# Optimization experiments

Measured on AMD Instinct MI355X. Metric: run time of the kernel, lower is better.

Reference implementation:

```python
import jax, jax.numpy as jnp
import numpy as np

INPUT_DIM = 1024
HIDDEN = 64
NUM_MEM = 8   # +1 shared slot -> 9 total
K = 2
SEQ = 256
BATCH = 32


def setup_inputs() -> dict:
    key = jax.random.key(0)
    ks = jax.random.split(key, 10)
    s = 1.0 / np.sqrt(INPUT_DIM)
    nm1 = NUM_MEM + 1
    return {
        "X": jax.random.normal(ks[0], (SEQ, BATCH, INPUT_DIM), jnp.float32),
        "M_0": jnp.zeros((BATCH, nm1, HIDDEN, HIDDEN), jnp.float32),
        "Wk_w": jax.random.uniform(ks[1], (HIDDEN * nm1, INPUT_DIM), jnp.float32, -s, s),
        "Wk_b": jax.random.uniform(ks[2], (HIDDEN * nm1,), jnp.float32, -s, s),
        "Wv_w": jax.random.uniform(ks[3], (HIDDEN * nm1, INPUT_DIM), jnp.float32, -s, s),
        "Wv_b": jax.random.uniform(ks[4], (HIDDEN * nm1,), jnp.float32, -s, s),
        "Wg_w": jax.random.uniform(ks[5], (NUM_MEM, INPUT_DIM), jnp.float32, -s, s),
        "Wg_b": jax.random.uniform(ks[6], (NUM_MEM,), jnp.float32, -s, s),
        "Wq_w": jax.random.uniform(ks[7], (HIDDEN, INPUT_DIM), jnp.float32, -s, s),
        "Wq_b": jax.random.uniform(ks[8], (HIDDEN,), jnp.float32, -s, s),
    }


def _mom_forward(X, M_0, Wk_w, Wk_b, Wv_w, Wv_b, Wg_w, Wg_b, Wq_w, Wq_b):
    B = X.shape[1]
    nm1 = NUM_MEM + 1
    b_idx = jnp.arange(B)[:, None]

    def step(M, x_t):
        # gating + top-k routing (sorted descending, like torch.topk)
        score = jax.nn.softmax(x_t @ Wg_w.T + Wg_b, axis=1)          # (B, NUM_MEM)
        m_scores, m_idx = jax.lax.top_k(score, K)                    # (B, K)
        idx_update = jnp.concatenate(
            [jnp.zeros((B, 1), jnp.int32), m_idx.astype(jnp.int32)], axis=1)  # (B, K+1)
        g = m_scores / jnp.sum(m_scores, axis=1, keepdims=True)     # (B, K)

        Mk = (x_t @ Wk_w.T + Wk_b).reshape(B, nm1, HIDDEN)          # (B, 9, H)
        Mv = (x_t @ Wv_w.T + Wv_b).reshape(B, nm1, HIDDEN)
        # only gather the K+1 routed outer products instead of all 9
        k_sel = jnp.take_along_axis(Mk, idx_update[:, :, None], axis=1)  # (B, K+1, H)
        v_sel = jnp.take_along_axis(Mv, idx_update[:, :, None], axis=1)
        src = k_sel[..., :, None] * v_sel[..., None, :]              # (B, K+1, H, H)
        M = M.at[b_idx, idx_update].add(src)                         # scatter-add (dupes accumulate)

        M_use = M[b_idx, m_idx]                                      # (B, K, H, H)
        M_out = jnp.einsum('bk,bkij->bij', g, M_use) + M[:, 0]       # add shared memory
        q = x_t @ Wq_w.T + Wq_b                                      # (B, H)
        o = jnp.einsum('bi,bij->bj', q, M_out)                       # (B, H)
        return M, o

    M_final, outputs = jax.lax.scan(step, M_0, X)
    return outputs, M_final


def reference(X, M_0, Wk_w, Wk_b, Wv_w, Wv_b, Wg_w, Wg_b, Wq_w, Wq_b):
    return _mom_forward(X, M_0, Wk_w, Wk_b, Wv_w, Wv_b, Wg_w, Wg_b, Wq_w, Wq_b)
```

## Files before the change

kernel.cpp:

```cpp
#include <hip/hip_runtime.h>
#include <stdint.h>

#define SEQ 256
#define BATCH 32
#define IN_DIM 1024
#define HID 64
#define NPAD 1280
#define ROWS (SEQ*BATCH)

#define XBF_OFF   0
#define DMH_OFF   0
#define WBF_OFF   16777216
#define BB_OFF    19398656
#define GATE_OFF  19403776
#define Y_OFF     19534848

#define NC 8
#define CHL 32

#define DM_CB_U32 18432

typedef __attribute__((ext_vector_type(8))) short short8;
typedef __attribute__((ext_vector_type(4))) float floatx4;

typedef const __attribute__((address_space(1))) unsigned int gas_u32;
typedef __attribute__((address_space(3))) unsigned int las_u32;
static __device__ __forceinline__ void gl_lds16(const void* g, void* l) {
  __builtin_amdgcn_global_load_lds((gas_u32*)g, (las_u32*)l, 16, 0, 0);
}

static __device__ __forceinline__ short f2bf(float f) {
  union { float f; uint32_t u; } a; a.f = f;
  uint32_t r = (a.u + 0x7FFFu + ((a.u >> 16) & 1u)) >> 16;
  return (short)r;
}
static __device__ __forceinline__ float bflo(uint32_t u){ return __uint_as_float(u << 16); }
static __device__ __forceinline__ float bfhi(uint32_t u){ return __uint_as_float(u & 0xffff0000u); }
static __device__ __forceinline__ float bfu(unsigned short us){ return __uint_as_float(((uint32_t)us) << 16); }

__global__ __launch_bounds__(256) void prep_gate_kernel(
    const float* __restrict__ X,
    const float* __restrict__ Wk, const float* __restrict__ bk,
    const float* __restrict__ Wv, const float* __restrict__ bv,
    const float* __restrict__ Wg, const float* __restrict__ bg,
    const float* __restrict__ Wq, const float* __restrict__ bq,
    short* __restrict__ Xbf, short* __restrict__ Wbf,
    float* __restrict__ bb, float4* __restrict__ gate)
{
  if (blockIdx.x < 2048) {
    int64_t idx = (int64_t)blockIdx.x * blockDim.x + threadIdx.x;
    int64_t stride = (int64_t)2048 * 256;
    const int64_t NX4 = (int64_t)ROWS * IN_DIM / 4;
    for (int64_t i = idx; i < NX4; i += stride) {
      float4 x = ((const float4*)X)[i];
      short4 s4;
      s4.x = f2bf(x.x); s4.y = f2bf(x.y); s4.z = f2bf(x.z); s4.w = f2bf(x.w);
      ((short4*)Xbf)[i] = s4;
    }
    const int64_t NW4 = (int64_t)NPAD * IN_DIM / 4;
    for (int64_t i = idx; i < NW4; i += stride) {
      int64_t e = i * 4;
      int r = (int)(e >> 10);
      int k = (int)(e & 1023);
      float4 x;
      if (r < 576)       x = *(const float4*)(Wk + (int64_t)r*1024 + k);
      else if (r < 1152) x = *(const float4*)(Wv + (int64_t)(r-576)*1024 + k);
      else if (r < 1216) x = *(const float4*)(Wq + (int64_t)(r-1152)*1024 + k);
      else               x = make_float4(0.f, 0.f, 0.f, 0.f);
      short4 s4;
      s4.x = f2bf(x.x); s4.y = f2bf(x.y); s4.z = f2bf(x.z); s4.w = f2bf(x.w);
      ((short4*)Wbf)[i] = s4;
    }
    for (int64_t i = idx; i < NPAD; i += stride) {
      int r = (int)i; float v;
      if (r < 576)       v = bk[r];
      else if (r < 1152) v = bv[r - 576];
      else if (r < 1216) v = bq[r - 1152];
      else               v = 0.f;
      bb[r] = v;
    }
  } else {
    const int lane = threadIdx.x & 63;
    const int row  = (blockIdx.x - 2048) * 4 + (threadIdx.x >> 6);
    const float* x = X + (int64_t)row * IN_DIM;

    float acc[8];
#pragma unroll
    for (int e = 0; e < 8; e++) acc[e] = 0.f;
#pragma unroll
    for (int i = 0; i < 4; i++) {
      const int off = i * 256 + lane * 4;
      float4 xv = *(const float4*)(x + off);
#pragma unroll
      for (int e = 0; e < 8; e++) {
        float4 wv = *(const float4*)(Wg + e * IN_DIM + off);
        acc[e] += xv.x * wv.x + xv.y * wv.y + xv.z * wv.z + xv.w * wv.w;
      }
    }
#pragma unroll
    for (int e = 0; e < 8; e++) {
#pragma unroll
      for (int m = 32; m >= 1; m >>= 1)
        acc[e] += __shfl_xor(acc[e], m);
      acc[e] += bg[e];
    }
    if (lane == 0) {
      int i0 = 0; float v0 = acc[0];
#pragma unroll
      for (int e = 1; e < 8; e++) if (acc[e] > v0) { v0 = acc[e]; i0 = e; }
      int i1 = -1; float v1 = -3.4e38f;
#pragma unroll
      for (int e = 0; e < 8; e++) if (e != i0 && acc[e] > v1) { v1 = acc[e]; i1 = e; }
      float e1 = __expf(v1 - v0);
      float inv = 1.f / (1.f + e1);
      gate[row] = make_float4(__int_as_float(i0), __int_as_float(i1), inv, e1 * inv);
    }
  }
}

__global__ __launch_bounds__(256) void gemm_kernel(
    const short* __restrict__ Xbf,
    const short* __restrict__ Wbf,
    const float* __restrict__ bb,
    float* __restrict__ Y)
{
  __shared__ short As[128 * 32];
  __shared__ short Bs[128 * 32];

  const int tid  = threadIdx.x;
  const int lane = tid & 63;
  const int wv   = tid >> 6;
  const int quad = lane >> 4;
  const int cl   = lane & 15;
  const int wm   = wv & 1;
  const int wn   = wv >> 1;
  const int m0 = blockIdx.y * 128;
  const int n0 = blockIdx.x * 128;

  const int srow = wv * 32 + (lane >> 2);
  const int scol = (lane & 3) * 8;
  const short* gA = Xbf + (int64_t)(m0 + srow) * IN_DIM + scol;
  const short* gB = Wbf + (int64_t)(n0 + srow) * IN_DIM + scol;
  short* lA = As + (wv * 32) * 32;
  short* lB = Bs + (wv * 32) * 32;

  floatx4 acc[4][4];
#pragma unroll
  for (int i = 0; i < 4; i++)
#pragma unroll
    for (int k = 0; k < 4; k++) acc[i][k] = (floatx4){0.f, 0.f, 0.f, 0.f};

  for (int ks = 0; ks < IN_DIM; ks += 32) {
    gl_lds16(gA + ks,                lA);
    gl_lds16(gA + 16 * IN_DIM + ks,  lA + 16 * 32);
    gl_lds16(gB + ks,                lB);
    gl_lds16(gB + 16 * IN_DIM + ks,  lB + 16 * 32);
    __syncthreads();

    short8 bfrag[4], afrag[4];
#pragma unroll
    for (int nt = 0; nt < 4; nt++)
      bfrag[nt] = *(const short8*)(&Bs[(wn * 64 + nt * 16 + cl) * 32 + quad * 8]);
#pragma unroll
    for (int mt = 0; mt < 4; mt++)
      afrag[mt] = *(const short8*)(&As[(wm * 64 + mt * 16 + cl) * 32 + quad * 8]);
#pragma unroll
    for (int mt = 0; mt < 4; mt++)
#pragma unroll
      for (int nt = 0; nt < 4; nt++)
        acc[mt][nt] = __builtin_amdgcn_mfma_f32_16x16x32_bf16(afrag[mt], bfrag[nt], acc[mt][nt], 0, 0, 0);
    __syncthreads();
  }

#pragma unroll
  for (int nt = 0; nt < 4; nt++) {
    const int col = n0 + wn * 64 + nt * 16 + cl;
    const float bias = bb[col];
#pragma unroll
    for (int mt = 0; mt < 4; mt++) {
#pragma unroll
      for (int r = 0; r < 4; r++) {
        int row = m0 + wm * 64 + mt * 16 + quad * 4 + r;
        Y[(int64_t)row * NPAD + col] = acc[mt][nt][r] + bias;
      }
    }
  }
}

__global__ __launch_bounds__(256) void mfma_chunk_kernel(
    const float* __restrict__ Y, const float4* __restrict__ gate,
    unsigned short* __restrict__ DMu, float* __restrict__ out)
{
  __shared__ uint32_t Qs[32 * 32];
  __shared__ uint32_t Ks[96 * 32];
  __shared__ unsigned short Kts[64 * 104];
  __shared__ unsigned short Vts[64 * 104];
  __shared__ unsigned short Ps[32 * 104];
  __shared__ float4 gl[32];
  __shared__ uint32_t su[96];

  const int blk = blockIdx.x;
  const int c   = blk & 7;
  const int b   = blk >> 3;
  const int tid = threadIdx.x;
  const int lane = tid & 63;
  const int wv  = tid >> 6;
  const int quad = lane >> 4;
  const int cl  = lane & 15;
  const int t0  = c * CHL;

  if (tid < 32) {
    float4 g = gate[(t0 + tid) * BATCH + b];
    gl[tid] = g;
    su[3 * tid]     = 0u;
    su[3 * tid + 1] = (uint32_t)__float_as_int(g.x);
    su[3 * tid + 2] = (uint32_t)__float_as_int(g.y);
  }
  __syncthreads();

  for (int idx = tid; idx < 3072; idx += 256) {
    const int e = idx >> 5, dd = idx & 31;
    const int s = (e * 171) >> 9;
    const int u = e - 3 * s;
    const int head = (u == 0) ? 0 : (int)su[3 * s + u];
    const float* Yr = Y + ((int64_t)(t0 + s) * BATCH + b) * NPAD;
    float f0 = Yr[head * 64 + 2 * dd], f1 = Yr[head * 64 + 2 * dd + 1];
    unsigned short b0 = (unsigned short)f2bf(f0), b1 = (unsigned short)f2bf(f1);
    Ks[e * 32 + dd] = (uint32_t)b0 | ((uint32_t)b1 << 16);
    Kts[(2 * dd) * 104 + e] = b0;
    Kts[(2 * dd + 1) * 104 + e] = b1;
    float v0 = Yr[576 + head * 64 + 2 * dd], v1 = Yr[576 + head * 64 + 2 * dd + 1];
    Vts[(2 * dd) * 104 + e] = (unsigned short)f2bf(v0);
    Vts[(2 * dd + 1) * 104 + e] = (unsigned short)f2bf(v1);
  }
  for (int idx = tid; idx < 1024; idx += 256) {
    const int s = idx >> 5, dd = idx & 31;
    const float* Yr = Y + ((int64_t)(t0 + s) * BATCH + b) * NPAD;
    Qs[s * 32 + dd] = ((uint32_t)(unsigned short)f2bf(Yr[1152 + 2 * dd])) |
                      (((uint32_t)(unsigned short)f2bf(Yr[1152 + 2 * dd + 1])) << 16);
  }
  __syncthreads();

  const unsigned short* Qu = (const unsigned short*)Qs;
  const unsigned short* Ku = (const unsigned short*)Ks;

#pragma unroll
  for (int q3 = 0; q3 < 3; q3++) {
    const int tileId = wv * 3 + q3;
    const int mt = tileId / 6, nt = tileId % 6;
    floatx4 acc = (floatx4){0.f, 0.f, 0.f, 0.f};
#pragma unroll
    for (int kc = 0; kc < 2; kc++) {
      short8 af = *(const short8*)(Qu + (mt * 16 + cl) * 64 + kc * 32 + quad * 8);
      short8 bf = *(const short8*)(Ku + (nt * 16 + cl) * 64 + kc * 32 + quad * 8);
      acc = __builtin_amdgcn_mfma_f32_16x16x32_bf16(af, bf, acc, 0, 0, 0);
    }
    const int e = nt * 16 + cl;
    const int s_e = (e * 171) >> 9;
    const int slot_e = (int)su[e];
#pragma unroll
    for (int r = 0; r < 4; r++) {
      const int t = mt * 16 + quad * 4 + r;
      float4 g = gl[t];
      const int i0t = __float_as_int(g.x), i1t = __float_as_int(g.y);
      float w = (slot_e == 0 ? 1.f : 0.f)
              + (slot_e == i0t ? g.z : 0.f)
              + (slot_e == i1t ? g.w : 0.f);
      w = (s_e <= t) ? w : 0.f;
      Ps[t * 104 + e] = (unsigned short)f2bf(w * acc[r]);
    }
  }
  __syncthreads();

#pragma unroll
  for (int q2 = 0; q2 < 2; q2++) {
    const int tileId = wv + q2 * 4;
    const int mt = tileId >> 2, nt = tileId & 3;
    floatx4 acc = (floatx4){0.f, 0.f, 0.f, 0.f};
#pragma unroll
    for (int kc = 0; kc < 3; kc++) {
      short8 af = *(const short8*)(Ps  + (mt * 16 + cl) * 104 + kc * 32 + quad * 8);
      short8 bf = *(const short8*)(Vts + (nt * 16 + cl) * 104 + kc * 32 + quad * 8);
      acc = __builtin_amdgcn_mfma_f32_16x16x32_bf16(af, bf, acc, 0, 0, 0);
    }
#pragma unroll
    for (int r = 0; r < 4; r++) {
      const int t = mt * 16 + quad * 4 + r, j = nt * 16 + cl;
      out[(int64_t)(t0 + t) * (BATCH * HID) + b * HID + j] = acc[r];
    }
  }

  uint32_t sreg[3][8];
#pragma unroll
  for (int kc = 0; kc < 3; kc++)
#pragma unroll
    for (int jj = 0; jj < 8; jj++)
      sreg[kc][jj] = su[kc * 32 + quad * 8 + jj];

  short8 afc[4][3];
#pragma unroll
  for (int mt = 0; mt < 4; mt++)
#pragma unroll
    for (int kc = 0; kc < 3; kc++)
      afc[mt][kc] = *(const short8*)(Kts + (mt * 16 + cl) * 104 + kc * 32 + quad * 8);

  unsigned short* dmb = DMu + ((int64_t)(c * 32 + b)) * 36864;
  union U8 { short8 s; uint32_t u[4]; };

  for (int mi = wv; mi < 9; mi += 4) {
    uint32_t md[3][4];
#pragma unroll
    for (int kc = 0; kc < 3; kc++)
#pragma unroll
      for (int p = 0; p < 4; p++)
        md[kc][p] = ((sreg[kc][2 * p]     == (uint32_t)mi) ? 0x0000ffffu : 0u) |
                    ((sreg[kc][2 * p + 1] == (uint32_t)mi) ? 0xffff0000u : 0u);
#pragma unroll
    for (int nt = 0; nt < 4; nt++) {
      short8 bm[3];
#pragma unroll
      for (int kc = 0; kc < 3; kc++) {
        U8 vv; vv.s = *(const short8*)(Vts + (nt * 16 + cl) * 104 + kc * 32 + quad * 8);
        vv.u[0] &= md[kc][0]; vv.u[1] &= md[kc][1];
        vv.u[2] &= md[kc][2]; vv.u[3] &= md[kc][3];
        bm[kc] = vv.s;
      }
#pragma unroll
      for (int mt = 0; mt < 4; mt++) {
        floatx4 acc = (floatx4){0.f, 0.f, 0.f, 0.f};
#pragma unroll
        for (int kc = 0; kc < 3; kc++)
          acc = __builtin_amdgcn_mfma_f32_16x16x32_bf16(afc[mt][kc], bm[kc], acc, 0, 0, 0);
#pragma unroll
        for (int r = 0; r < 4; r++) {
          const int i = mt * 16 + quad * 4 + r, j = nt * 16 + cl;
          dmb[mi * 4096 + i * 64 + j] = (unsigned short)f2bf(acc[r]);
        }
      }
    }
  }
}

__global__ void prefix_kernel(const float* __restrict__ M0, uint32_t* __restrict__ DMh,
                              float* __restrict__ out, int nc)
{
  int64_t e = (int64_t)blockIdx.x * blockDim.x + threadIdx.x;
  int b = (int)(e / DM_CB_U32);
  int r = (int)(e % DM_CB_U32);
  int m = r >> 11, rem = r & 2047, i = rem >> 5, jp = rem & 31;
  int64_t f32i = (int64_t)b * 36864 + m * 4096 + i * 64 + jp * 2;
  float run0 = M0[f32i], run1 = M0[f32i + 1];
  for (int cc = 0; cc < nc; cc++) {
    int64_t idx = ((int64_t)(cc * 32 + b)) * DM_CB_U32 + r;
    uint32_t u = DMh[idx];
    DMh[idx] = ((uint32_t)(unsigned short)f2bf(run0)) |
               (((uint32_t)(unsigned short)f2bf(run1)) << 16);
    run0 += bflo(u); run1 += bfhi(u);
  }
  *(float2*)(out + (int64_t)SEQ * BATCH * HID + f32i) = make_float2(run0, run1);
}

__global__ __launch_bounds__(256) void corr_kernel(
    const float* __restrict__ Y, const float4* __restrict__ gate,
    const uint32_t* __restrict__ DMh, float* __restrict__ out)
{
  __shared__ uint32_t Msb32[9 * 64 * 16];
  __shared__ float2 qb[32 * 32];
  __shared__ float4 gl[32];
  unsigned short* Msb = (unsigned short*)Msb32;
  const int blk = blockIdx.x;
  const int c   = blk & 7;
  const int jh  = (blk >> 3) & 1;
  const int b   = blk >> 4;
  const int tid = threadIdx.x;
  const int t0  = c * CHL;

  if (tid < 32) gl[tid] = gate[(t0 + tid) * BATCH + b];
#pragma unroll
  for (int k = 0; k < 4; k++) {
    int f = tid + 256 * k;
    int t = f >> 5, p = f & 31;
    qb[t * 32 + p] = *(const float2*)(Y + ((int64_t)(t0 + t) * BATCH + b) * NPAD + 1152 + 2 * p);
  }
  const uint32_t* dmb = DMh + ((int64_t)(c * 32 + b)) * DM_CB_U32;
#pragma unroll
  for (int k = 0; k < 36; k++) {
    int f = tid + 256 * k;
    int m = f >> 10, rem = f & 1023, i = rem >> 4, p = rem & 15;
    Msb32[(m * 64 + i) * 16 + p] = dmb[m * 2048 + i * 32 + jh * 16 + p];
  }
  __syncthreads();

  const int jj = tid & 31;
  const int tg = tid >> 5;
#pragma unroll
  for (int tt = 0; tt < 4; tt++) {
    const int t = tt * 8 + tg;
    float4 g = gl[t];
    const int i0 = __float_as_int(g.x), i1 = __float_as_int(g.y);
    const float g0 = g.z, g1 = g.w;
    float acc = 0.f;
#pragma unroll 8
    for (int i2 = 0; i2 < 32; i2++) {
      float2 qq = qb[t * 32 + i2];
      int ia = 2 * i2;
      float m0a = bfu(Msb[(0  * 64 + ia) * 32 + jj]);
      float m0b = bfu(Msb[(0  * 64 + ia + 1) * 32 + jj]);
      float maa = bfu(Msb[(i0 * 64 + ia) * 32 + jj]);
      float mab = bfu(Msb[(i0 * 64 + ia + 1) * 32 + jj]);
      float mba = bfu(Msb[(i1 * 64 + ia) * 32 + jj]);
      float mbb = bfu(Msb[(i1 * 64 + ia + 1) * 32 + jj]);
      acc += qq.x * (m0a + g0 * maa + g1 * mba);
      acc += qq.y * (m0b + g0 * mab + g1 * mbb);
    }
    float* op = out + (int64_t)(t0 + t) * (BATCH * HID) + b * HID + jh * 32 + jj;
    *op += acc;
  }
}

extern "C" void kernel_launch(void* const* d_in, const int* in_sizes, int n_in,
                              void* d_out, int out_size, void* d_ws, size_t ws_size,
                              hipStream_t stream)
{
  const float* X  = (const float*)d_in[0];
  const float* M0 = (const float*)d_in[1];
  const float* Wk = (const float*)d_in[2];
  const float* bk = (const float*)d_in[3];
  const float* Wv = (const float*)d_in[4];
  const float* bv = (const float*)d_in[5];
  const float* Wg = (const float*)d_in[6];
  const float* bg = (const float*)d_in[7];
  const float* Wq = (const float*)d_in[8];
  const float* bq = (const float*)d_in[9];

  char* ws = (char*)d_ws;
  short*          Xbf  = (short*)(ws + XBF_OFF);
  short*          Wbf  = (short*)(ws + WBF_OFF);
  float*          bb   = (float*)(ws + BB_OFF);
  float4*         gate = (float4*)(ws + GATE_OFF);
  float*          Y    = (float*)(ws + Y_OFF);
  uint32_t*       DMh  = (uint32_t*)(ws + DMH_OFF);
  unsigned short* DMu  = (unsigned short*)(ws + DMH_OFF);
  float*          out  = (float*)d_out;

  prep_gate_kernel<<<4096, 256, 0, stream>>>(X, Wk, bk, Wv, bv, Wg, bg, Wq, bq,
                                             Xbf, Wbf, bb, gate);
  dim3 gg(NPAD / 128, ROWS / 128);
  gemm_kernel<<<gg, 256, 0, stream>>>(Xbf, Wbf, bb, Y);
  mfma_chunk_kernel<<<32 * NC, 256, 0, stream>>>(Y, gate, DMu, out);
  prefix_kernel<<<(32 * DM_CB_U32) / 256, 256, 0, stream>>>(M0, DMh, out, NC);
  corr_kernel<<<32 * NC * 2, 256, 0, stream>>>(Y, gate, DMh, out);
}
```

Measured before the change: 182.2 us.

## Double-buffer GEMM LDS tiles, remap block order, widen chunk kernel to 512 threads

The GEMM now double-buffers its A/B shared-memory tiles, so the global-to-LDS load for the next K slice is issued before the MFMAs on the current slice run. It also launches a 1D grid whose block index is remapped so consecutive blocks spread across XCDs. The chunk kernel moves to 512 threads (8 waves), with its tile loops redistributed so each wave does less serial work. The trade-offs are double the LDS per GEMM block, which may lower occupancy, and an uneven split of the 9 memory slots across 8 waves in the chunk kernel.

Result: slower. 187.7 us (+3.0%).

```diff
diff --git a/kernel.cpp b/kernel.cpp
--- a/kernel.cpp
+++ b/kernel.cpp
@@ -124,8 +124,8 @@
     const float* __restrict__ bb,
     float* __restrict__ Y)
 {
-  __shared__ short As[128 * 32];
-  __shared__ short Bs[128 * 32];
+  __shared__ short As[2][128 * 32];
+  __shared__ short Bs[2][128 * 32];
 
   const int tid  = threadIdx.x;
   const int lane = tid & 63;
@@ -134,15 +134,22 @@
   const int cl   = lane & 15;
   const int wm   = wv & 1;
   const int wn   = wv >> 1;
-  const int m0 = blockIdx.y * 128;
-  const int n0 = blockIdx.x * 128;
+
+  const int h   = blockIdx.x;
+  const int id2 = (h & 7) * 80 + (h >> 3);
+  const int by  = id2 / 10;
+  const int bx  = id2 - by * 10;
+  const int m0  = by * 128;
+  const int n0  = bx * 128;
 
   const int srow = wv * 32 + (lane >> 2);
   const int scol = (lane & 3) * 8;
   const short* gA = Xbf + (int64_t)(m0 + srow) * IN_DIM + scol;
   const short* gB = Wbf + (int64_t)(n0 + srow) * IN_DIM + scol;
-  short* lA = As + (wv * 32) * 32;
-  short* lB = Bs + (wv * 32) * 32;
+  short* lA0 = As[0] + (wv * 32) * 32;
+  short* lA1 = As[1] + (wv * 32) * 32;
+  short* lB0 = Bs[0] + (wv * 32) * 32;
+  short* lB1 = Bs[1] + (wv * 32) * 32;
 
   floatx4 acc[4][4];
 #pragma unroll
@@ -150,27 +157,42 @@
 #pragma unroll
     for (int k = 0; k < 4; k++) acc[i][k] = (floatx4){0.f, 0.f, 0.f, 0.f};
 
-  for (int ks = 0; ks < IN_DIM; ks += 32) {
-    gl_lds16(gA + ks,                lA);
-    gl_lds16(gA + 16 * IN_DIM + ks,  lA + 16 * 32);
-    gl_lds16(gB + ks,                lB);
-    gl_lds16(gB + 16 * IN_DIM + ks,  lB + 16 * 32);
+#define STAGE(LA, LB, KS) do {                          \
+    gl_lds16(gA + (KS),               (LA));            \
+    gl_lds16(gA + 16 * IN_DIM + (KS), (LA) + 16 * 32);  \
+    gl_lds16(gB + (KS),               (LB));            \
+    gl_lds16(gB + 16 * IN_DIM + (KS), (LB) + 16 * 32);  \
+  } while (0)
+
+#define COMPUTE(B) do {                                                         \
+    short8 bfrag[4], afrag[4];                                                  \
+    _Pragma("unroll")                                                           \
+    for (int nt = 0; nt < 4; nt++)                                              \
+      bfrag[nt] = *(const short8*)(&Bs[B][(wn * 64 + nt * 16 + cl) * 32 + quad * 8]); \
+    _Pragma("unroll")                                                           \
+    for (int mt = 0; mt < 4; mt++)                                              \
+      afrag[mt] = *(const short8*)(&As[B][(wm * 64 + mt * 16 + cl) * 32 + quad * 8]); \
+    _Pragma("unroll")                                                           \
+    for (int mt = 0; mt < 4; mt++)                                              \
+      _Pragma("unroll")                                                         \
+      for (int nt = 0; nt < 4; nt++)                                            \
+        acc[mt][nt] = __builtin_amdgcn_mfma_f32_16x16x32_bf16(afrag[mt], bfrag[nt], acc[mt][nt], 0, 0, 0); \
+  } while (0)
+
+  STAGE(lA0, lB0, 0);
+  __syncthreads();
+
+  for (int ks = 0; ks < IN_DIM; ks += 64) {
+    STAGE(lA1, lB1, ks + 32);
+    COMPUTE(0);
     __syncthreads();
-
-    short8 bfrag[4], afrag[4];
-#pragma unroll
-    for (int nt = 0; nt < 4; nt++)
-      bfrag[nt] = *(const short8*)(&Bs[(wn * 64 + nt * 16 + cl) * 32 + quad * 8]);
-#pragma unroll
-    for (int mt = 0; mt < 4; mt++)
-      afrag[mt] = *(const short8*)(&As[(wm * 64 + mt * 16 + cl) * 32 + quad * 8]);
-#pragma unroll
-    for (int mt = 0; mt < 4; mt++)
-#pragma unroll
-      for (int nt = 0; nt < 4; nt++)
-        acc[mt][nt] = __builtin_amdgcn_mfma_f32_16x16x32_bf16(afrag[mt], bfrag[nt], acc[mt][nt], 0, 0, 0);
+    if (ks + 64 < IN_DIM)
+      STAGE(lA0, lB0, ks + 64);
+    COMPUTE(1);
     __syncthreads();
   }
+#undef STAGE
+#undef COMPUTE
 
 #pragma unroll
   for (int nt = 0; nt < 4; nt++) {
@@ -187,7 +209,7 @@
   }
 }
 
-__global__ __launch_bounds__(256) void mfma_chunk_kernel(
+__global__ __launch_bounds__(512) void mfma_chunk_kernel(
     const float* __restrict__ Y, const float4* __restrict__ gate,
     unsigned short* __restrict__ DMu, float* __restrict__ out)
 {
@@ -218,7 +240,7 @@
   }
   __syncthreads();
 
-  for (int idx = tid; idx < 3072; idx += 256) {
+  for (int idx = tid; idx < 3072; idx += 512) {
     const int e = idx >> 5, dd = idx & 31;
     const int s = (e * 171) >> 9;
     const int u = e - 3 * s;
@@ -233,7 +255,7 @@
     Vts[(2 * dd) * 104 + e] = (unsigned short)f2bf(v0);
     Vts[(2 * dd + 1) * 104 + e] = (unsigned short)f2bf(v1);
   }
-  for (int idx = tid; idx < 1024; idx += 256) {
+  for (int idx = tid; idx < 1024; idx += 512) {
     const int s = idx >> 5, dd = idx & 31;
     const float* Yr = Y + ((int64_t)(t0 + s) * BATCH + b) * NPAD;
     Qs[s * 32 + dd] = ((uint32_t)(unsigned short)f2bf(Yr[1152 + 2 * dd])) |
@@ -244,9 +266,7 @@
   const unsigned short* Qu = (const unsigned short*)Qs;
   const unsigned short* Ku = (const unsigned short*)Ks;
 
-#pragma unroll
-  for (int q3 = 0; q3 < 3; q3++) {
-    const int tileId = wv * 3 + q3;
+  for (int tileId = wv; tileId < 12; tileId += 8) {
     const int mt = tileId / 6, nt = tileId % 6;
     floatx4 acc = (floatx4){0.f, 0.f, 0.f, 0.f};
 #pragma unroll
@@ -272,9 +292,8 @@
   }
   __syncthreads();
 
-#pragma unroll
-  for (int q2 = 0; q2 < 2; q2++) {
-    const int tileId = wv + q2 * 4;
+  {
+    const int tileId = wv;
     const int mt = tileId >> 2, nt = tileId & 3;
     floatx4 acc = (floatx4){0.f, 0.f, 0.f, 0.f};
 #pragma unroll
@@ -307,7 +326,7 @@
   unsigned short* dmb = DMu + ((int64_t)(c * 32 + b)) * 36864;
   union U8 { short8 s; uint32_t u[4]; };
 
-  for (int mi = wv; mi < 9; mi += 4) {
+  for (int mi = wv; mi < 9; mi += 8) {
     uint32_t md[3][4];
 #pragma unroll
     for (int kc = 0; kc < 3; kc++)
@@ -445,9 +464,8 @@
 
   prep_gate_kernel<<<4096, 256, 0, stream>>>(X, Wk, bk, Wv, bv, Wg, bg, Wq, bq,
                                              Xbf, Wbf, bb, gate);
-  dim3 gg(NPAD / 128, ROWS / 128);
-  gemm_kernel<<<gg, 256, 0, stream>>>(Xbf, Wbf, bb, Y);
-  mfma_chunk_kernel<<<32 * NC, 256, 0, stream>>>(Y, gate, DMu, out);
+  gemm_kernel<<<640, 256, 0, stream>>>(Xbf, Wbf, bb, Y);
+  mfma_chunk_kernel<<<32 * NC, 512, 0, stream>>>(Y, gate, DMu, out);
   prefix_kernel<<<(32 * DM_CB_U32) / 256, 256, 0, stream>>>(M0, DMh, out, NC);
   corr_kernel<<<32 * NC * 2, 256, 0, stream>>>(Y, gate, DMh, out);
 }
```
